# Kernel optimization log

Measured on AMD Instinct MI355X. Metric: run time of the kernel, lower is better.

Reference implementation:

```python
import jax, jax.numpy as jnp
import numpy as np
from jax import lax

B, C, T = 64, 122, 500
COUT, D, H, FF, L = 64, 128, 8, 256, 2
NSUB, NCLS = 13, 4
EPS = 1e-5


def _gelu(x):
    return jax.nn.gelu(x, approximate=False)  # torch nn.GELU default (erf)


def _bn(x, g, b, m, v):
    # eval-mode BatchNorm1d over channel dim of [N, C, T]
    scale = (g / jnp.sqrt(v + EPS))[None, :, None]
    return (x - m[None, :, None]) * scale + b[None, :, None]


def _ln(x, g, b):
    mu = x.mean(-1, keepdims=True)
    var = ((x - mu) ** 2).mean(-1, keepdims=True)
    return (x - mu) / jnp.sqrt(var + EPS) * g + b


def _conv1d(x, w, b, pad):
    y = lax.conv_general_dilated(x, w, (1,), [(pad, pad)], dimension_numbers=('NCH', 'OIH', 'NCH'))
    return y + b[None, :, None]


def forward(x, subject_ids, conv1_w, conv1_b, bn1_g, bn1_b, bn1_m, bn1_v,
            conv2_w, conv2_b, bn2_g, bn2_b, bn2_m, bn2_v,
            proj_w, proj_b, elec_emb,
            qkv_w, qkv_b, out_w, out_b, ln1_g, ln1_b,
            ff1_w, ff1_b, ff2_w, ff2_b, ln2_g, ln2_b,
            heads_w, heads_b):
    bsz = x.shape[0]
    h = x.reshape(bsz * C, 1, T)                               # [B*C, 1, T]
    h = _gelu(_bn(_conv1d(h, conv1_w, conv1_b, 4), bn1_g, bn1_b, bn1_m, bn1_v))
    h = h.reshape(bsz * C, COUT, T // 2, 2).max(-1)            # MaxPool1d(2)
    h = _gelu(_bn(_conv1d(h, conv2_w, conv2_b, 2), bn2_g, bn2_b, bn2_m, bn2_v))
    h = h.mean(-1)                                             # AdaptiveAvgPool1d(1)
    tok = h @ proj_w.T + proj_b                                # [B*C, D]
    tok = tok.reshape(bsz, C, D) + elec_emb[:, :C, :]
    dh = D // H
    inv_sqrt_dh = 1.0 / float(np.sqrt(dh))
    for l in range(L):  # post-norm TransformerEncoderLayer, gelu activation
        qkv = jnp.einsum('bsd,ed->bse', tok, qkv_w[l]) + qkv_b[l]
        q, k, v = jnp.split(qkv, 3, axis=-1)
        q = q.reshape(bsz, C, H, dh)
        k = k.reshape(bsz, C, H, dh)
        v = v.reshape(bsz, C, H, dh)
        att = jax.nn.softmax(jnp.einsum('bqhd,bkhd->bhqk', q, k) * inv_sqrt_dh, axis=-1)
        ctx = jnp.einsum('bhqk,bkhd->bqhd', att, v).reshape(bsz, C, D)
        tok = _ln(tok + ctx @ out_w[l].T + out_b[l], ln1_g[l], ln1_b[l])
        ff = _gelu(tok @ ff1_w[l].T + ff1_b[l]) @ ff2_w[l].T + ff2_b[l]
        tok = _ln(tok + ff, ln2_g[l], ln2_b[l])
    pooled = tok.mean(axis=1)                                  # [B, D]
    # per-subject head routing == gather subject's weight/bias, batched matvec
    hw = heads_w[subject_ids]                                  # [B, NCLS, D]
    hb = heads_b[subject_ids]                                  # [B, NCLS]
    return jnp.einsum('bd,bcd->bc', pooled, hw) + hb


def setup_inputs() -> dict:
    key = jax.random.key(0)
    ks = jax.random.split(key, 16)
    def n(i, shape, s=0.02):
        return jax.random.normal(ks[i], shape, jnp.float32) * s
    return {
        'x': jax.random.normal(ks[0], (B, C, T), jnp.float32),
        'subject_ids': jax.random.randint(ks[1], (B,), 0, NSUB),
        'conv1_w': n(2, (COUT, 1, 9), 0.3), 'conv1_b': jnp.zeros((COUT,), jnp.float32),
        'bn1_g': jnp.ones((COUT,), jnp.float32), 'bn1_b': jnp.zeros((COUT,), jnp.float32),
        'bn1_m': jnp.zeros((COUT,), jnp.float32), 'bn1_v': jnp.ones((COUT,), jnp.float32),
        'conv2_w': n(3, (COUT, COUT, 5), 0.05), 'conv2_b': jnp.zeros((COUT,), jnp.float32),
        'bn2_g': jnp.ones((COUT,), jnp.float32), 'bn2_b': jnp.zeros((COUT,), jnp.float32),
        'bn2_m': jnp.zeros((COUT,), jnp.float32), 'bn2_v': jnp.ones((COUT,), jnp.float32),
        'proj_w': n(4, (D, COUT), 0.05), 'proj_b': jnp.zeros((D,), jnp.float32),
        'elec_emb': n(5, (1, C, D), 0.02),
        'qkv_w': n(6, (L, 3 * D, D), 0.05), 'qkv_b': jnp.zeros((L, 3 * D), jnp.float32),
        'out_w': n(7, (L, D, D), 0.05), 'out_b': jnp.zeros((L, D), jnp.float32),
        'ln1_g': jnp.ones((L, D), jnp.float32), 'ln1_b': jnp.zeros((L, D), jnp.float32),
        'ff1_w': n(8, (L, FF, D), 0.05), 'ff1_b': jnp.zeros((L, FF), jnp.float32),
        'ff2_w': n(9, (L, D, FF), 0.05), 'ff2_b': jnp.zeros((L, D), jnp.float32),
        'ln2_g': jnp.ones((L, D), jnp.float32), 'ln2_b': jnp.zeros((L, D), jnp.float32),
        'heads_w': n(10, (NSUB, NCLS, D), 0.05), 'heads_b': jnp.zeros((NSUB, NCLS), jnp.float32),
    }


def reference(x, subject_ids, conv1_w, conv1_b, bn1_g, bn1_b, bn1_m, bn1_v,
              conv2_w, conv2_b, bn2_g, bn2_b, bn2_m, bn2_v,
              proj_w, proj_b, elec_emb,
              qkv_w, qkv_b, out_w, out_b, ln1_g, ln1_b,
              ff1_w, ff1_b, ff2_w, ff2_b, ln2_g, ln2_b,
              heads_w, heads_b):
    return forward(x, subject_ids, conv1_w, conv1_b, bn1_g, bn1_b, bn1_m, bn1_v,
                   conv2_w, conv2_b, bn2_g, bn2_b, bn2_m, bn2_v,
                   proj_w, proj_b, elec_emb,
                   qkv_w, qkv_b, out_w, out_b, ln1_g, ln1_b,
                   ff1_w, ff1_b, ff2_w, ff2_b, ln2_g, ln2_b,
                   heads_w, heads_b)
```

## Files before the change

kernel.cpp:

```cpp
#include <hip/hip_runtime.h>
#include <hip/hip_fp16.h>
#include <hip/hip_bf16.h>
#include <math.h>

#define BB 64
#define CC 122
#define TT 500
#define NCOUT 64
#define DD 128
#define HHEADS 8
#define FFDIM 256
#define NLAYER 2
#define EPS 1e-5f
#define SEQ (BB*CC)

#define WS_W2T     0u
#define WS_S1      20480u
#define WS_SH1     20544u
#define WS_S2      20608u
#define WS_SH2     20672u
#define WS_WBF     20736u
#define WS_TOK     151808u
#define WS_QKVB    1151232u
#define WS_VTB     2150656u
#define WS_GTAB    2674944u
#define WS_W1S     2675968u

#define WB_QKV  0u
#define WB_OUT  98304u
#define WB_FF1  131072u
#define WB_FF2  196608u

typedef __attribute__((ext_vector_type(8))) short bf16x8;
typedef __attribute__((ext_vector_type(4))) float f32x4;

__device__ __forceinline__ unsigned short f2bf(float f) {
    unsigned int u = __float_as_uint(f);
    unsigned int r = u + 0x7FFFu + ((u >> 16) & 1u);
    return (unsigned short)(r >> 16);
}

__device__ __forceinline__ float gelu_fast(float x) {
    float z = fabsf(x) * 0.70710678118654752f;
    float t = __builtin_amdgcn_rcpf(fmaf(0.3275911f, z, 1.0f));
    float p = fmaf(fmaf(fmaf(fmaf(1.061405429f, t, -1.453152027f), t,
                             1.421413741f), t, -0.284496736f), t, 0.254829592f);
    float e = __expf(-z * z);
    float erf_abs = fmaf(-p * t, e, 1.0f);
    float erf_x = copysignf(erf_abs, x);
    return 0.5f * x * (1.0f + erf_x);
}

__device__ __forceinline__ float gelu_tab(float x, const unsigned* __restrict__ gt) {
    float p = fmaf(x, 32.0f, 256.0f);
    p = fminf(fmaxf(p, 0.0f), 511.999f);
    int i = (int)p;
    float fr = p - (float)i;
    unsigned u = gt[i];
    __half2 h2 = *(__half2*)&u;
    float v0 = __half2float(h2.x);
    float d  = __half2float(h2.y);
    return fmaf(fr, d, v0);
}

__global__ void prep_kernel(const float* __restrict__ conv1_w, const float* __restrict__ conv1_b,
                            const float* __restrict__ bn1_g, const float* __restrict__ bn1_b,
                            const float* __restrict__ bn1_m, const float* __restrict__ bn1_v,
                            const float* __restrict__ conv2_w, const float* __restrict__ conv2_b,
                            const float* __restrict__ bn2_g, const float* __restrict__ bn2_b,
                            const float* __restrict__ bn2_m, const float* __restrict__ bn2_v,
                            const float* __restrict__ qkv_w, const float* __restrict__ out_w,
                            const float* __restrict__ ff1_w, const float* __restrict__ ff2_w,
                            float* __restrict__ ws) {
    int idx = blockIdx.x * blockDim.x + threadIdx.x;
    if (idx < 20480) {
        int ci = idx & 63; int co = (idx >> 6) & 63; int kk = idx >> 12;
        unsigned short* wt = (unsigned short*)(ws + WS_W2T);
        wt[idx] = f2bf(conv2_w[(co*64 + ci)*5 + kk]);
    } else if (idx < 20544) {
        int i = idx - 20480;
        float s = bn1_g[i] * rsqrtf(bn1_v[i] + EPS);
        ws[WS_S1 + i] = s;
        ws[WS_SH1 + i] = (conv1_b[i] - bn1_m[i]) * s + bn1_b[i];
    } else if (idx < 20608) {
        int i = idx - 20544;
        float s = bn2_g[i] * rsqrtf(bn2_v[i] + EPS);
        ws[WS_S2 + i] = s;
        ws[WS_SH2 + i] = (conv2_b[i] - bn2_m[i]) * s + bn2_b[i];
    } else if (idx < 282752) {
        int r = idx - 20608;
        unsigned short* wbf = (unsigned short*)(ws + WS_WBF);
        float v;
        if (r < 98304)       v = qkv_w[r];
        else if (r < 131072) v = out_w[r - 98304];
        else if (r < 196608) v = ff1_w[r - 131072];
        else                 v = ff2_w[r - 196608];
        wbf[r] = f2bf(v);
    } else if (idx < 283264) {
        int i = idx - 282752;
        float x0 = (i - 256) * 0.03125f;
        float x1 = x0 + 0.03125f;
        float g0 = 0.5f*x0*(1.0f + erff(x0*0.70710678118654752f));
        float g1 = 0.5f*x1*(1.0f + erff(x1*0.70710678118654752f));
        __half hv = __float2half_rn(g0);
        __half hd = __float2half_rn(g1 - g0);
        unsigned short uv = *(unsigned short*)&hv;
        unsigned short ud = *(unsigned short*)&hd;
        ((unsigned*)(ws + WS_GTAB))[i] = (unsigned)uv | ((unsigned)ud << 16);
    } else if (idx < 285312) {
        int i = idx - 283264;
        int co = i >> 5, k = i & 31;
        unsigned short* w1s = (unsigned short*)(ws + WS_W1S);
        float s = bn1_g[co] * rsqrtf(bn1_v[co] + EPS);
        w1s[i] = (k < 9) ? f2bf(conv1_w[co*9 + k] * s) : (unsigned short)0;
    }
}

__global__ __launch_bounds__(256, 4) void conv_kernel(const float* __restrict__ x,
            const float* __restrict__ proj_w, const float* __restrict__ proj_b,
            const float* __restrict__ elec,
            const float* __restrict__ wsr, float* __restrict__ tok) {
    __shared__ __align__(16) unsigned short h1s[264*64];
    __shared__ __align__(16) unsigned short xbf[544];
    __shared__ __align__(16) unsigned gtab[512];
    __shared__ float part[256];
    __shared__ float mean_l[64];
    int n = blockIdx.x;
    int c = n % CC;
    int tid = threadIdx.x;
    const float* xg = x + (size_t)n * TT;

    for (int i = tid; i < 544; i += 256) {
        unsigned short v = 0;
        if (i >= 4 && i < 504) v = f2bf(xg[i-4]);
        xbf[i] = v;
    }
    if (tid < 128) {
        ((uint4*)gtab)[tid] = ((const uint4*)(wsr + WS_GTAB))[tid];
    }
    for (int idx = tid; idx < 14*64; idx += 256) {
        int rr = idx >> 6;
        int r = (rr < 2) ? rr : (rr - 2 + 252);
        h1s[r*64 + (idx & 63)] = 0;
    }
    __syncthreads();

    int lane = tid & 63;
    int w = tid >> 6;
    int ln15 = lane & 15, lg = lane >> 4;

    {
        const unsigned short* w1s = (const unsigned short*)(wsr + WS_W1S);
        bf16x8 b1f[4];
        float sh1v[4];
#pragma unroll
        for (int nt = 0; nt < 4; nt++) {
            int co = nt*16 + ln15;
            b1f[nt] = *(const bf16x8*)&w1s[co*32 + lg*8];
            sh1v[nt] = wsr[WS_SH1 + co];
        }
        for (int mi = 0; mi < 8; mi++) {
            int mt = w*8 + mi;
            int t = mt*16 + ln15;
            short e[8];
#pragma unroll
            for (int j = 0; j < 8; j++) e[j] = (short)xbf[t + lg*8 + j];
            bf16x8 af = {e[0],e[1],e[2],e[3],e[4],e[5],e[6],e[7]};
#pragma unroll
            for (int nt = 0; nt < 4; nt++) {
                f32x4 cacc = __builtin_amdgcn_mfma_f32_16x16x32_bf16(af, b1f[nt],
                                (f32x4){0.f,0.f,0.f,0.f}, 0, 0, 0);
                float g0 = gelu_tab(cacc[0] + sh1v[nt], gtab);
                float g1 = gelu_tab(cacc[1] + sh1v[nt], gtab);
                float g2 = gelu_tab(cacc[2] + sh1v[nt], gtab);
                float g3 = gelu_tab(cacc[3] + sh1v[nt], gtab);
                int tpA = mt*8 + lg*2;
                if (tpA < 250) {
                    int co = nt*16 + ln15;
                    union { __hip_bfloat162 b; unsigned u; } pk;
                    pk.b = __float22bfloat162_rn(make_float2(fmaxf(g0, g1), fmaxf(g2, g3)));
                    int r = tpA + 2;
                    int cp = (co >> 3) ^ (r & 7);
                    h1s[r*64 + cp*8 + (co & 7)] = (unsigned short)(pk.u & 0xffffu);
                    int r2 = r + 1;
                    int cp2 = (co >> 3) ^ (r2 & 7);
                    h1s[r2*64 + cp2*8 + (co & 7)] = (unsigned short)(pk.u >> 16);
                }
            }
        }
    }
    __syncthreads();

    const unsigned short* wt = (const unsigned short*)(wsr + WS_W2T);
    f32x4 acc[4][4];
#pragma unroll
    for (int mi = 0; mi < 4; mi++)
#pragma unroll
        for (int nt = 0; nt < 4; nt++) acc[mi][nt] = (f32x4){0.f, 0.f, 0.f, 0.f};

    const unsigned short* wbase = wt + ln15*64 + lg*8;
#pragma unroll
    for (int kk = 0; kk < 5; kk++) {
#pragma unroll
        for (int s = 0; s < 2; s++) {
            bf16x8 bfv[4];
#pragma unroll
            for (int nt = 0; nt < 4; nt++)
                bfv[nt] = *(const bf16x8*)(wbase + kk*4096 + nt*1024 + s*32);
#pragma unroll
            for (int mi = 0; mi < 4; mi++) {
                int r = (w*4 + mi)*16 + ln15 + kk;
                int cp = (s*4 + lg) ^ (r & 7);
                bf16x8 af = *(const bf16x8*)&h1s[r*64 + cp*8];
#pragma unroll
                for (int nt = 0; nt < 4; nt++)
                    acc[mi][nt] = __builtin_amdgcn_mfma_f32_16x16x32_bf16(af, bfv[nt], acc[mi][nt], 0, 0, 0);
            }
        }
    }

#pragma unroll
    for (int nt = 0; nt < 4; nt++) {
        int co2 = nt*16 + ln15;
        float sc = wsr[WS_S2 + co2], sh = wsr[WS_SH2 + co2];
        float p = 0.f;
#pragma unroll
        for (int mi = 0; mi < 4; mi++) {
            int tbase = (w*4 + mi)*16 + lg*4;
#pragma unroll
            for (int i = 0; i < 4; i++) {
                if (tbase + i < 250)
                    p += gelu_tab(fmaf(acc[mi][nt][i], sc, sh), gtab);
            }
        }
        p += __shfl_down(p, 32, 64);
        p += __shfl_down(p, 16, 64);
        if (lane < 16) part[w*64 + co2] = p;
    }
    __syncthreads();
    if (tid < 64) {
        mean_l[tid] = (part[tid] + part[64+tid] + part[128+tid] + part[192+tid]) * (1.0f/250.0f);
    }
    __syncthreads();

    if (tid < DD) {
        int d = tid;
        float a = proj_b[d] + elec[c*DD + d];
#pragma unroll 8
        for (int o = 0; o < 64; o++) a = fmaf(mean_l[o], proj_w[d*64 + o], a);
        tok[(size_t)n * DD + d] = a;
    }
}

__global__ __launch_bounds__(256) void qkv_gemm(const float* __restrict__ Aptr,
        const unsigned short* __restrict__ Bbf,
        const float* __restrict__ bias,
        unsigned short* __restrict__ qkvb,
        unsigned short* __restrict__ vtb) {
    const int tid = threadIdx.x;
    const int m0 = blockIdx.x * 32;
    const int y  = blockIdx.y;
    const int n0 = y * 128;
    __shared__ __align__(16) unsigned short As[32*128];

    const float* A = Aptr + (size_t)m0 * 128;
    for (int i = tid; i < 1024; i += 256) {
        int m = i >> 5; int kq = (i & 31)*4;
        float4 v = *(const float4*)(A + m*128 + kq);
        int cp = (kq >> 3) ^ (m & 15);
        short4 s4 = make_short4((short)f2bf(v.x), (short)f2bf(v.y),
                                (short)f2bf(v.z), (short)f2bf(v.w));
        *(short4*)&As[m*128 + cp*8 + (kq & 7)] = s4;
    }
    __syncthreads();

    const int lane = tid & 63, w = tid >> 6;
    const int ln15 = lane & 15, lg = lane >> 4;
    f32x4 acc[2][2];
#pragma unroll
    for (int mi = 0; mi < 2; mi++)
#pragma unroll
        for (int ni = 0; ni < 2; ni++) acc[mi][ni] = (f32x4){0.f, 0.f, 0.f, 0.f};

    const unsigned short* Bb = Bbf + (size_t)n0 * 128;
#pragma unroll
    for (int kt = 0; kt < 4; kt++) {
        bf16x8 af[2], bfv[2];
#pragma unroll
        for (int mi = 0; mi < 2; mi++) {
            int m = mi*16 + ln15;
            int cp = (kt*4 + lg) ^ (m & 15);
            af[mi] = *(const bf16x8*)&As[m*128 + cp*8];
        }
#pragma unroll
        for (int ni = 0; ni < 2; ni++) {
            int nn = (w*2 + ni)*16 + ln15;
            bfv[ni] = *(const bf16x8*)&Bb[(size_t)nn*128 + kt*32 + lg*8];
        }
#pragma unroll
        for (int mi = 0; mi < 2; mi++)
#pragma unroll
            for (int ni = 0; ni < 2; ni++)
                acc[mi][ni] = __builtin_amdgcn_mfma_f32_16x16x32_bf16(af[mi], bfv[ni], acc[mi][ni], 0, 0, 0);
    }

#pragma unroll
    for (int mi = 0; mi < 2; mi++)
#pragma unroll
        for (int ni = 0; ni < 2; ni++) {
            int nloc = (w*2 + ni)*16 + ln15;
            float bb = bias[n0 + nloc];
#pragma unroll
            for (int i = 0; i < 4; i++) {
                int ml = mi*16 + lg*4 + i;
                int nrow = m0 + ml;
                unsigned short us = f2bf(acc[mi][ni][i] + bb);
                if (y < 2) {
                    qkvb[(size_t)nrow*256 + n0 + nloc] = us;
                } else {
                    int bq = nrow / 122;
                    int j  = nrow - bq*122;
                    vtb[((size_t)(bq*128 + nloc))*128 + j] = us;
                }
            }
        }
}

__global__ __launch_bounds__(512) void attn_tail(
        const unsigned short* __restrict__ qkvb,
        const unsigned short* __restrict__ vtb,
        const unsigned short* __restrict__ outW, const float* __restrict__ outb,
        float* __restrict__ tok,
        const float* __restrict__ ln1g, const float* __restrict__ ln1b,
        const unsigned short* __restrict__ B1, const float* __restrict__ b1,
        const unsigned short* __restrict__ B2, const float* __restrict__ b2,
        const float* __restrict__ ln2g, const float* __restrict__ ln2b) {
    __shared__ float Cs[32*129];
    __shared__ __align__(16) unsigned short Pregion[8*16*128];
    __shared__ __align__(16) unsigned short ctxs[32*128];

    const int tid = threadIdx.x;
    const int blk = blockIdx.x;
    const int b = blk >> 2, mq = blk & 3;
    const int m0l = mq * 32;
    const int lane = tid & 63, w = tid >> 6;
    const int ln15 = lane & 15, lg = lane >> 4;

    const unsigned short* qb = qkvb + (size_t)b * 122 * 256;
    unsigned short* Pw = Pregion + w * 2048;

    {
        const int h = w;
#pragma unroll
        for (int mt = 0; mt < 2; mt++) {
            int mrow = m0l + mt*16 + ln15;
            int gr = (mrow < 122) ? mrow : 121;
            bf16x8 af = {0,0,0,0,0,0,0,0};
            if (lg < 2) af = *(const bf16x8*)(qb + gr*256 + h*16 + lg*8);
            f32x4 S[8];
#pragma unroll
            for (int nt = 0; nt < 8; nt++) {
                int j = nt*16 + ln15;
                int gj = (j < 122) ? j : 121;
                bf16x8 bv = {0,0,0,0,0,0,0,0};
                if (lg < 2) bv = *(const bf16x8*)(qb + gj*256 + 128 + h*16 + lg*8);
                S[nt] = __builtin_amdgcn_mfma_f32_16x16x32_bf16(af, bv,
                            (f32x4){0.f,0.f,0.f,0.f}, 0, 0, 0);
            }
            float sm[4];
#pragma unroll
            for (int i = 0; i < 4; i++) {
                float m_ = -1e30f;
#pragma unroll
                for (int nt = 0; nt < 8; nt++) {
                    float v = S[nt][i] * 0.25f;
                    if (nt == 7 && ln15 >= 10) v = -1e30f;
                    S[nt][i] = v;
                    m_ = fmaxf(m_, v);
                }
                m_ = fmaxf(m_, __shfl_xor(m_, 1, 64));
                m_ = fmaxf(m_, __shfl_xor(m_, 2, 64));
                m_ = fmaxf(m_, __shfl_xor(m_, 4, 64));
                m_ = fmaxf(m_, __shfl_xor(m_, 8, 64));
                float s_ = 0.f;
#pragma unroll
                for (int nt = 0; nt < 8; nt++) {
                    float e = __expf(S[nt][i] - m_);
                    S[nt][i] = e;
                    s_ += e;
                }
                s_ += __shfl_xor(s_, 1, 64);
                s_ += __shfl_xor(s_, 2, 64);
                s_ += __shfl_xor(s_, 4, 64);
                s_ += __shfl_xor(s_, 8, 64);
                sm[i] = s_;
            }
#pragma unroll
            for (int nt = 0; nt < 8; nt++)
#pragma unroll
                for (int i = 0; i < 4; i++) {
                    int rp = lg*4 + i;
                    int j = nt*16 + ln15;
                    int cp = (j >> 3) ^ rp;
                    Pw[rp*128 + cp*8 + (j & 7)] = f2bf(S[nt][i]);
                }
            f32x4 cacc = (f32x4){0.f,0.f,0.f,0.f};
#pragma unroll
            for (int kt = 0; kt < 4; kt++) {
                bf16x8 bv = *(const bf16x8*)(vtb + ((size_t)(b*128 + h*16 + ln15))*128 + kt*32 + lg*8);
                int m = ln15;
                int cp = (kt*4 + lg) ^ m;
                bf16x8 ap = *(const bf16x8*)&Pw[m*128 + cp*8];
                cacc = __builtin_amdgcn_mfma_f32_16x16x32_bf16(ap, bv, cacc, 0, 0, 0);
            }
#pragma unroll
            for (int i = 0; i < 4; i++) {
                float inv = __builtin_amdgcn_rcpf(sm[i]);
                int rp = mt*16 + lg*4 + i;
                int ccol = h*16 + ln15;
                int cp = (ccol >> 3) ^ (rp & 15);
                ctxs[rp*128 + cp*8 + (ccol & 7)] = f2bf(cacc[i] * inv);
            }
        }
    }
    __syncthreads();

    {
        f32x4 acc[2];
#pragma unroll
        for (int mi = 0; mi < 2; mi++) acc[mi] = (f32x4){0.f,0.f,0.f,0.f};
        int nn = w*16 + ln15;
#pragma unroll
        for (int kt = 0; kt < 4; kt++) {
            bf16x8 bv = *(const bf16x8*)&outW[(size_t)nn*128 + kt*32 + lg*8];
#pragma unroll
            for (int mi = 0; mi < 2; mi++) {
                int m = mi*16 + ln15;
                int cp = (kt*4 + lg) ^ (m & 15);
                bf16x8 afm = *(const bf16x8*)&ctxs[m*128 + cp*8];
                acc[mi] = __builtin_amdgcn_mfma_f32_16x16x32_bf16(afm, bv, acc[mi], 0, 0, 0);
            }
        }
        float bb = outb[nn];
#pragma unroll
        for (int mi = 0; mi < 2; mi++)
#pragma unroll
            for (int i = 0; i < 4; i++) {
                int ml = mi*16 + lg*4 + i;
                int mrow = m0l + ml;
                int grow = b*122 + ((mrow < 122) ? mrow : 121);
                Cs[ml*129 + nn] = acc[mi][i] + bb + tok[(size_t)grow*128 + nn];
            }
    }
    __syncthreads();

    unsigned short* ln1buf = Pregion;
    unsigned short* Hs = Pregion + 4096;
    {
        int r = tid >> 4, sub = tid & 15;
        float s1 = 0.f, s2 = 0.f;
#pragma unroll
        for (int j = 0; j < 8; j++) {
            float vv = Cs[r*129 + sub*8 + j];
            s1 += vv; s2 += vv*vv;
        }
        s1 += __shfl_xor(s1, 1, 64); s2 += __shfl_xor(s2, 1, 64);
        s1 += __shfl_xor(s1, 2, 64); s2 += __shfl_xor(s2, 2, 64);
        s1 += __shfl_xor(s1, 4, 64); s2 += __shfl_xor(s2, 4, 64);
        s1 += __shfl_xor(s1, 8, 64); s2 += __shfl_xor(s2, 8, 64);
        float mu = s1 * (1.0f/128.0f);
        float var = s2 * (1.0f/128.0f) - mu*mu;
        float rstd = rsqrtf(var + EPS);
#pragma unroll
        for (int j = 0; j < 8; j++) {
            int nloc = sub*8 + j;
            float vv = (Cs[r*129 + nloc] - mu) * rstd * ln1g[nloc] + ln1b[nloc];
            Cs[r*129 + nloc] = vv;
            int cp = (nloc >> 3) ^ (r & 15);
            ln1buf[r*128 + cp*8 + (nloc & 7)] = f2bf(vv);
        }
    }
    __syncthreads();

    {
        f32x4 acc1[2][2];
#pragma unroll
        for (int mi = 0; mi < 2; mi++)
#pragma unroll
            for (int ni = 0; ni < 2; ni++) acc1[mi][ni] = (f32x4){0.f,0.f,0.f,0.f};
#pragma unroll
        for (int kt = 0; kt < 4; kt++) {
            bf16x8 afm[2];
#pragma unroll
            for (int mi = 0; mi < 2; mi++) {
                int m = mi*16 + ln15;
                int cp = (kt*4 + lg) ^ (m & 15);
                afm[mi] = *(const bf16x8*)&ln1buf[m*128 + cp*8];
            }
#pragma unroll
            for (int ni = 0; ni < 2; ni++) {
                int nn = (w*2 + ni)*16 + ln15;
                bf16x8 bv = *(const bf16x8*)&B1[(size_t)nn*128 + kt*32 + lg*8];
#pragma unroll
                for (int mi = 0; mi < 2; mi++)
                    acc1[mi][ni] = __builtin_amdgcn_mfma_f32_16x16x32_bf16(afm[mi], bv, acc1[mi][ni], 0, 0, 0);
            }
        }
#pragma unroll
        for (int ni = 0; ni < 2; ni++) {
            int nn = (w*2 + ni)*16 + ln15;
            float bb = b1[nn];
#pragma unroll
            for (int mi = 0; mi < 2; mi++)
#pragma unroll
                for (int i = 0; i < 4; i++) {
                    int m = mi*16 + lg*4 + i;
                    float v = gelu_fast(acc1[mi][ni][i] + bb);
                    int cp = (nn >> 3) ^ (m & 15);
                    Hs[m*256 + cp*8 + (nn & 7)] = f2bf(v);
                }
        }
    }
    __syncthreads();

    {
        f32x4 acc2[2];
#pragma unroll
        for (int mi = 0; mi < 2; mi++) acc2[mi] = (f32x4){0.f,0.f,0.f,0.f};
        int nn = w*16 + ln15;
#pragma unroll
        for (int kt = 0; kt < 8; kt++) {
            bf16x8 bv = *(const bf16x8*)&B2[(size_t)nn*256 + kt*32 + lg*8];
#pragma unroll
            for (int mi = 0; mi < 2; mi++) {
                int m = mi*16 + ln15;
                int cp = (kt*4 + lg) ^ (m & 15);
                bf16x8 afm = *(const bf16x8*)&Hs[m*256 + cp*8];
                acc2[mi] = __builtin_amdgcn_mfma_f32_16x16x32_bf16(afm, bv, acc2[mi], 0, 0, 0);
            }
        }
        float bb = b2[nn];
#pragma unroll
        for (int mi = 0; mi < 2; mi++)
#pragma unroll
            for (int i = 0; i < 4; i++) {
                int ml = mi*16 + lg*4 + i;
                Cs[ml*129 + nn] = acc2[mi][i] + bb + Cs[ml*129 + nn];
            }
    }
    __syncthreads();

    {
        int r = tid >> 4, sub = tid & 15;
        float s1 = 0.f, s2 = 0.f;
#pragma unroll
        for (int j = 0; j < 8; j++) {
            float vv = Cs[r*129 + sub*8 + j];
            s1 += vv; s2 += vv*vv;
        }
        s1 += __shfl_xor(s1, 1, 64); s2 += __shfl_xor(s2, 1, 64);
        s1 += __shfl_xor(s1, 2, 64); s2 += __shfl_xor(s2, 2, 64);
        s1 += __shfl_xor(s1, 4, 64); s2 += __shfl_xor(s2, 4, 64);
        s1 += __shfl_xor(s1, 8, 64); s2 += __shfl_xor(s2, 8, 64);
        float mu = s1 * (1.0f/128.0f);
        float var = s2 * (1.0f/128.0f) - mu*mu;
        float rstd = rsqrtf(var + EPS);
        if (m0l + r < 122) {
#pragma unroll
            for (int j = 0; j < 8; j++) {
                int nloc = sub*8 + j;
                float vv = (Cs[r*129 + nloc] - mu) * rstd * ln2g[nloc] + ln2b[nloc];
                tok[((size_t)(b*122 + m0l + r))*128 + nloc] = vv;
            }
        }
    }
}

__global__ __launch_bounds__(128) void final_kernel(const float* __restrict__ tok,
        const int* __restrict__ sid,
        const float* __restrict__ hw, const float* __restrict__ hb,
        float* __restrict__ outp) {
    __shared__ float pool[DD];
    int b = blockIdx.x, tid = threadIdx.x;
    float s = 0.f;
    for (int c2 = 0; c2 < CC; c2++) s += tok[((size_t)b*CC + c2)*DD + tid];
    pool[tid] = s * (1.0f/(float)CC);
    __syncthreads();
    if (tid < 4) {
        int sb = sid[b];
        const float* w = hw + ((size_t)sb*4 + tid)*DD;
        float a = hb[sb*4 + tid];
#pragma unroll 8
        for (int d = 0; d < DD; d++) a = fmaf(pool[d], w[d], a);
        outp[b*4 + tid] = a;
    }
}

extern "C" void kernel_launch(void* const* d_in, const int* in_sizes, int n_in,
                              void* d_out, int out_size, void* d_ws, size_t ws_size,
                              hipStream_t stream) {
    const float* x       = (const float*)d_in[0];
    const int*   sid     = (const int*)  d_in[1];
    const float* conv1_w = (const float*)d_in[2];
    const float* conv1_b = (const float*)d_in[3];
    const float* bn1_g   = (const float*)d_in[4];
    const float* bn1_b   = (const float*)d_in[5];
    const float* bn1_m   = (const float*)d_in[6];
    const float* bn1_v   = (const float*)d_in[7];
    const float* conv2_w = (const float*)d_in[8];
    const float* conv2_b = (const float*)d_in[9];
    const float* bn2_g   = (const float*)d_in[10];
    const float* bn2_b   = (const float*)d_in[11];
    const float* bn2_m   = (const float*)d_in[12];
    const float* bn2_v   = (const float*)d_in[13];
    const float* proj_w  = (const float*)d_in[14];
    const float* proj_b  = (const float*)d_in[15];
    const float* elec    = (const float*)d_in[16];
    const float* qkv_w   = (const float*)d_in[17];
    const float* qkv_b   = (const float*)d_in[18];
    const float* out_w   = (const float*)d_in[19];
    const float* out_b   = (const float*)d_in[20];
    const float* ln1_g   = (const float*)d_in[21];
    const float* ln1_b   = (const float*)d_in[22];
    const float* ff1_w   = (const float*)d_in[23];
    const float* ff1_b   = (const float*)d_in[24];
    const float* ff2_w   = (const float*)d_in[25];
    const float* ff2_b   = (const float*)d_in[26];
    const float* ln2_g   = (const float*)d_in[27];
    const float* ln2_b   = (const float*)d_in[28];
    const float* heads_w = (const float*)d_in[29];
    const float* heads_b = (const float*)d_in[30];
    float* ws = (float*)d_ws;
    const unsigned short* wbf = (const unsigned short*)(ws + WS_WBF);
    unsigned short* qkvb = (unsigned short*)(ws + WS_QKVB);
    unsigned short* vtb  = (unsigned short*)(ws + WS_VTB);

    prep_kernel<<<(285312 + 255)/256, 256, 0, stream>>>(
        conv1_w, conv1_b, bn1_g, bn1_b, bn1_m, bn1_v,
        conv2_w, conv2_b, bn2_g, bn2_b, bn2_m, bn2_v,
        qkv_w, out_w, ff1_w, ff2_w, ws);

    conv_kernel<<<SEQ, 256, 0, stream>>>(x, proj_w, proj_b, elec, ws, ws + WS_TOK);

    for (int l = 0; l < NLAYER; l++) {
        qkv_gemm<<<dim3(244,3), 256, 0, stream>>>(
            ws + WS_TOK, wbf + WB_QKV + l*49152, qkv_b + l*384, qkvb, vtb);
        attn_tail<<<BB*4, 512, 0, stream>>>(
            qkvb, vtb,
            wbf + WB_OUT + l*16384, out_b + l*128,
            ws + WS_TOK, ln1_g + l*128, ln1_b + l*128,
            wbf + WB_FF1 + l*32768, ff1_b + l*256,
            wbf + WB_FF2 + l*32768, ff2_b + l*128,
            ln2_g + l*128, ln2_b + l*128);
    }

    final_kernel<<<BB, 128, 0, stream>>>(ws + WS_TOK, sid, heads_w, heads_b, (float*)d_out);
}
```

Before: 419.5 us.

## Fuse layer-2 QKV projection into layer-1 attention tail kernel

The layer-1 attention/FFN tail kernel now also computes the next layer's QKV projection from its LayerNorm output, staging it as bf16 in shared memory and writing Q/K and transposed V into a second set of buffers. This removes one qkv_gemm launch and the re-read of the token tensor from global memory. The tail kernel gains extra MFMA work, registers and a barrier, which may affect occupancy. Separate output buffers avoid a race with blocks of the same batch that are still reading the layer-1 QKV.

```diff
diff --git a/kernel.cpp b/kernel.cpp
--- a/kernel.cpp
+++ b/kernel.cpp
@@ -25,6 +25,8 @@
 #define WS_VTB     2150656u
 #define WS_GTAB    2674944u
 #define WS_W1S     2675968u
+#define WS_QKVB2   2676992u
+#define WS_VTB2    3676416u
 
 #define WB_QKV  0u
 #define WB_OUT  98304u
@@ -334,7 +336,10 @@
         const float* __restrict__ ln1g, const float* __restrict__ ln1b,
         const unsigned short* __restrict__ B1, const float* __restrict__ b1,
         const unsigned short* __restrict__ B2, const float* __restrict__ b2,
-        const float* __restrict__ ln2g, const float* __restrict__ ln2b) {
+        const float* __restrict__ ln2g, const float* __restrict__ ln2b,
+        const unsigned short* __restrict__ Bq, const float* __restrict__ bq,
+        unsigned short* __restrict__ qkvb_o, unsigned short* __restrict__ vtb_o,
+        int do_qkv) {
     __shared__ float Cs[32*129];
     __shared__ __align__(16) unsigned short Pregion[8*16*128];
     __shared__ __align__(16) unsigned short ctxs[32*128];
@@ -565,13 +570,65 @@
         float mu = s1 * (1.0f/128.0f);
         float var = s2 * (1.0f/128.0f) - mu*mu;
         float rstd = rsqrtf(var + EPS);
-        if (m0l + r < 122) {
-#pragma unroll
-            for (int j = 0; j < 8; j++) {
-                int nloc = sub*8 + j;
-                float vv = (Cs[r*129 + nloc] - mu) * rstd * ln2g[nloc] + ln2b[nloc];
+        bool rowok = (m0l + r < 122);
+#pragma unroll
+        for (int j = 0; j < 8; j++) {
+            int nloc = sub*8 + j;
+            float vv = (Cs[r*129 + nloc] - mu) * rstd * ln2g[nloc] + ln2b[nloc];
+            if (rowok)
                 tok[((size_t)(b*122 + m0l + r))*128 + nloc] = vv;
-            }
+            if (do_qkv) {
+                int cp = (nloc >> 3) ^ (r & 15);
+                Pregion[r*128 + cp*8 + (nloc & 7)] = f2bf(vv);
+            }
+        }
+    }
+
+    if (do_qkv) {
+        __syncthreads();
+        const unsigned short* qbuf = Pregion;
+        f32x4 accq[2][3];
+#pragma unroll
+        for (int mi = 0; mi < 2; mi++)
+#pragma unroll
+            for (int ni = 0; ni < 3; ni++) accq[mi][ni] = (f32x4){0.f,0.f,0.f,0.f};
+#pragma unroll
+        for (int kt = 0; kt < 4; kt++) {
+            bf16x8 afm[2];
+#pragma unroll
+            for (int mi = 0; mi < 2; mi++) {
+                int m = mi*16 + ln15;
+                int cp = (kt*4 + lg) ^ (m & 15);
+                afm[mi] = *(const bf16x8*)&qbuf[m*128 + cp*8];
+            }
+#pragma unroll
+            for (int ni = 0; ni < 3; ni++) {
+                int e = w*48 + ni*16 + ln15;
+                bf16x8 bv = *(const bf16x8*)&Bq[(size_t)e*128 + kt*32 + lg*8];
+#pragma unroll
+                for (int mi = 0; mi < 2; mi++)
+                    accq[mi][ni] = __builtin_amdgcn_mfma_f32_16x16x32_bf16(afm[mi], bv, accq[mi][ni], 0, 0, 0);
+            }
+        }
+#pragma unroll
+        for (int ni = 0; ni < 3; ni++) {
+            int e = w*48 + ni*16 + ln15;
+            float bb = bq[e];
+#pragma unroll
+            for (int mi = 0; mi < 2; mi++)
+#pragma unroll
+                for (int i = 0; i < 4; i++) {
+                    int ml = mi*16 + lg*4 + i;
+                    int mrow = m0l + ml;
+                    if (mrow < 122) {
+                        unsigned short us = f2bf(accq[mi][ni][i] + bb);
+                        int nrow = b*122 + mrow;
+                        if (e < 256)
+                            qkvb_o[(size_t)nrow*256 + e] = us;
+                        else
+                            vtb_o[((size_t)(b*128 + (e - 256)))*128 + mrow] = us;
+                    }
+                }
         }
     }
 }
@@ -632,8 +689,10 @@
     const float* heads_b = (const float*)d_in[30];
     float* ws = (float*)d_ws;
     const unsigned short* wbf = (const unsigned short*)(ws + WS_WBF);
-    unsigned short* qkvb = (unsigned short*)(ws + WS_QKVB);
-    unsigned short* vtb  = (unsigned short*)(ws + WS_VTB);
+    unsigned short* qkvb  = (unsigned short*)(ws + WS_QKVB);
+    unsigned short* vtb   = (unsigned short*)(ws + WS_VTB);
+    unsigned short* qkvb2 = (unsigned short*)(ws + WS_QKVB2);
+    unsigned short* vtb2  = (unsigned short*)(ws + WS_VTB2);
 
     prep_kernel<<<(285312 + 255)/256, 256, 0, stream>>>(
         conv1_w, conv1_b, bn1_g, bn1_b, bn1_m, bn1_v,
@@ -642,17 +701,26 @@
 
     conv_kernel<<<SEQ, 256, 0, stream>>>(x, proj_w, proj_b, elec, ws, ws + WS_TOK);
 
-    for (int l = 0; l < NLAYER; l++) {
-        qkv_gemm<<<dim3(244,3), 256, 0, stream>>>(
-            ws + WS_TOK, wbf + WB_QKV + l*49152, qkv_b + l*384, qkvb, vtb);
-        attn_tail<<<BB*4, 512, 0, stream>>>(
-            qkvb, vtb,
-            wbf + WB_OUT + l*16384, out_b + l*128,
-            ws + WS_TOK, ln1_g + l*128, ln1_b + l*128,
-            wbf + WB_FF1 + l*32768, ff1_b + l*256,
-            wbf + WB_FF2 + l*32768, ff2_b + l*128,
-            ln2_g + l*128, ln2_b + l*128);
-    }
+    qkv_gemm<<<dim3(244,3), 256, 0, stream>>>(
+        ws + WS_TOK, wbf + WB_QKV, qkv_b, qkvb, vtb);
+
+    attn_tail<<<BB*4, 512, 0, stream>>>(
+        qkvb, vtb,
+        wbf + WB_OUT, out_b,
+        ws + WS_TOK, ln1_g, ln1_b,
+        wbf + WB_FF1, ff1_b,
+        wbf + WB_FF2, ff2_b,
+        ln2_g, ln2_b,
+        wbf + WB_QKV + 49152, qkv_b + 384, qkvb2, vtb2, 1);
+
+    attn_tail<<<BB*4, 512, 0, stream>>>(
+        qkvb2, vtb2,
+        wbf + WB_OUT + 16384, out_b + 128,
+        ws + WS_TOK, ln1_g + 128, ln1_b + 128,
+        wbf + WB_FF1 + 32768, ff1_b + 256,
+        wbf + WB_FF2 + 32768, ff2_b + 128,
+        ln2_g + 128, ln2_b + 128,
+        wbf + WB_QKV, qkv_b, qkvb2, vtb2, 0);
 
     final_kernel<<<BB, 128, 0, stream>>>(ws + WS_TOK, sid, heads_w, heads_b, (float*)d_out);
 }
```

New measurement: 418.2 us. About the same (-0.3%).
